# Optimization experiments

Hardware: AMD Instinct MI355X
Metric: run time of the kernel (lower is better)

## Reference

```python
import jax, jax.numpy as jnp
import numpy as np
import math

DIM_IN, DIM_OUT, DIM_HID = 128, 128, 512
DEPTH, HEADS, DIM_HEAD, MLP = 6, 8, 64, 2048
INNER = HEADS * DIM_HEAD  # 512


def _inorm(t, eps=1e-5):
    # torch InstanceNorm1d on ((b h), n, d): normalize over last (spatial) dim, biased var, no affine
    m = jnp.mean(t, axis=-1, keepdims=True)
    v = jnp.mean((t - m) ** 2, axis=-1, keepdims=True)
    return (t - m) * jax.lax.rsqrt(v + eps)


def _layernorm(t, g, b, eps=1e-5):
    m = jnp.mean(t, axis=-1, keepdims=True)
    v = jnp.mean((t - m) ** 2, axis=-1, keepdims=True)
    return (t - m) * jax.lax.rsqrt(v + eps) * g + b


def _pos_encoding(n, d):
    pos = jnp.arange(n, dtype=jnp.float32)[:, None]
    div = jnp.exp(jnp.arange(0, d, 2, dtype=jnp.float32) * (-math.log(10000.0) / d))
    pe = jnp.zeros((n, d), dtype=jnp.float32)
    pe = pe.at[:, 0::2].set(jnp.sin(pos * div))
    pe = pe.at[:, 1::2].set(jnp.cos(pos * div))
    return pe


def setup_inputs() -> dict:
    key = jax.random.key(0)
    ks = jax.random.split(key, 16)
    s = 0.02
    return {
        "x": jax.random.normal(ks[0], (4, 64, 4096, 2), jnp.float32),
        "W_emb": jax.random.normal(ks[1], (DIM_IN, DIM_HID), jnp.float32) * s,
        "b_emb": jnp.zeros((DIM_HID,), jnp.float32),
        "ln_g": jnp.ones((DEPTH, DIM_HID), jnp.float32),
        "ln_b": jnp.zeros((DEPTH, DIM_HID), jnp.float32),
        "Wqkv": jax.random.normal(ks[2], (DEPTH, DIM_HID, 3 * INNER), jnp.float32) * s,
        "Wout": jax.random.normal(ks[3], (DEPTH, INNER, DIM_HID), jnp.float32) * s,
        "b_out": jnp.zeros((DEPTH, DIM_HID), jnp.float32),
        "W1": jax.random.normal(ks[4], (DEPTH, DIM_HID, 2 * MLP), jnp.float32) * s,
        "b1": jnp.zeros((DEPTH, 2 * MLP), jnp.float32),
        "W2": jax.random.normal(ks[5], (DEPTH, MLP, DIM_HID), jnp.float32) * s,
        "b2": jnp.zeros((DEPTH, DIM_HID), jnp.float32),
        "Wd": jax.random.normal(ks[6], (DIM_HID, DIM_OUT), jnp.float32) * s,
        "bd": jnp.zeros((DIM_OUT,), jnp.float32),
    }


def reference(x, W_emb, b_emb, ln_g, ln_b, Wqkv, Wout, b_out, W1, b1, W2, b2, Wd, bd):
    b, t, n, c = x.shape
    h = x.transpose(0, 2, 1, 3).reshape(b, n, t * c)        # [b, n, dim_in]
    h = (h @ W_emb + b_emb) * math.sqrt(DIM_HID)
    h = h + _pos_encoding(n, DIM_HID)[None]                 # positional encoding (dropout=0)
    inv_n = 1.0 / n
    for i in range(DEPTH):
        # PreNorm(LinearAttention) + residual
        y = _layernorm(h, ln_g[i], ln_b[i])
        qkv = y @ Wqkv[i]                                   # [b, n, 3*inner]
        q, k, v = jnp.split(qkv, 3, axis=-1)
        sp = lambda z: z.reshape(b, n, HEADS, DIM_HEAD).transpose(0, 2, 1, 3)  # b h n d
        q, k, v = sp(q), sp(k), sp(v)
        k, v = _inorm(k), _inorm(v)                         # galerkin: norm K and V
        dots = jnp.einsum('bhnd,bhne->bhde', k, v)          # k^T v: O(n) attention
        o = jnp.einsum('bhnd,bhde->bhne', q, dots) * inv_n
        o = o.transpose(0, 2, 1, 3).reshape(b, n, INNER)
        h = o @ Wout[i] + b_out[i] + h
        # FeedForward (no PreNorm in galerkin branch) + residual
        f = h @ W1[i] + b1[i]
        f = jax.nn.gelu(f[..., :MLP], approximate=False) * f[..., MLP:]
        h = f @ W2[i] + b2[i] + h
    out = h @ Wd + bd                                       # [b, n, dim_out]
    return out.transpose(0, 2, 1).reshape(b, -1, 1)         # [b, dim_out*n, 1]
```

## Files before the change

kernel.cpp:

```cpp
#include <hip/hip_runtime.h>
#include <hip/hip_bf16.h>
#include <stdint.h>
#include <math.h>


typedef _Float16 f16x8 __attribute__((ext_vector_type(8)));
typedef float f32x4 __attribute__((ext_vector_type(4)));
typedef unsigned short u16x8 __attribute__((ext_vector_type(8)));
typedef unsigned short u16;

#define SEQ 4096
#define NTOK 16384
#define HID 512
#define RSCL 256.0f
#define RSCLI (1.0f/256.0f)

__device__ __forceinline__ float wred(float x) {
#pragma unroll
  for (int off = 32; off; off >>= 1) x += __shfl_xor(x, off);
  return x;
}

__device__ __forceinline__ u16 f2h(float v) {
  _Float16 h = (_Float16)v;
  return __builtin_bit_cast(u16, h);
}
__device__ __forceinline__ float h2f(u16 u) {
  return (float)__builtin_bit_cast(_Float16, u);
}

__device__ __forceinline__ void gload16(const void* g, void* l) {
  __builtin_amdgcn_global_load_lds(
      reinterpret_cast<const __attribute__((address_space(1))) int*>(
          reinterpret_cast<uintptr_t>(g)),
      reinterpret_cast<__attribute__((address_space(3))) int*>(
          reinterpret_cast<uintptr_t>(l)),
      16, 0, 0);
}

__global__ __launch_bounds__(256) void k_transpose(const float* __restrict__ src,
                                                   u16* __restrict__ dst,
                                                   int K, int N) {
  int d = blockIdx.z;
  const float* s = src + (size_t)d * K * N;
  u16* o = dst + (size_t)d * N * K;
  int k0 = blockIdx.x * 64, n0 = blockIdx.y * 64;
  __shared__ float tile[64][65];
  int t = threadIdx.x, c = t & 63, r4 = t >> 6;
#pragma unroll
  for (int i = 0; i < 16; ++i) {
    int r = i * 4 + r4;
    tile[r][c] = s[(size_t)(k0 + r) * N + n0 + c];
  }
  __syncthreads();
#pragma unroll
  for (int i = 0; i < 16; ++i) {
    int r = i * 4 + r4;
    o[(size_t)(n0 + r) * K + k0 + c] = f2h(tile[c][r]);
  }
}

__global__ __launch_bounds__(256) void k_packx(const float* __restrict__ x,
                                               u16* __restrict__ XP) {
  int idx = blockIdx.x * 256 + threadIdx.x;
  int k = idx & 127, row = idx >> 7;
  int b = row >> 12, n = row & 4095;
  int tt = k >> 1, c = k & 1;
  XP[idx] = f2h(x[(((size_t)(b * 64 + tt)) * SEQ + n) * 2 + c]);
}

__global__ __launch_bounds__(256) void k_ln(const float* __restrict__ H,
                                            const float* __restrict__ G,
                                            const float* __restrict__ B,
                                            u16* __restrict__ Y) {
  int t = threadIdx.x, lane = t & 63;
  int row = blockIdx.x * 4 + (t >> 6);
  const float4* h4 = (const float4*)(H + (size_t)row * HID);
  float4 a = h4[lane * 2], b = h4[lane * 2 + 1];
  float v[8] = {a.x, a.y, a.z, a.w, b.x, b.y, b.z, b.w};
  float s = v[0] + v[1] + v[2] + v[3] + v[4] + v[5] + v[6] + v[7];
  s = wred(s);
  float m = s * (1.0f / 512.0f);
  float q = 0.f;
#pragma unroll
  for (int i = 0; i < 8; ++i) {
    v[i] -= m;
    q += v[i] * v[i];
  }
  q = wred(q);
  float rs = rsqrtf(q * (1.0f / 512.0f) + 1e-5f);
  const float4* g4 = (const float4*)G;
  const float4* b4 = (const float4*)B;
  float4 g1 = g4[lane * 2], g2 = g4[lane * 2 + 1];
  float4 e1 = b4[lane * 2], e2 = b4[lane * 2 + 1];
  float gg[8] = {g1.x, g1.y, g1.z, g1.w, g2.x, g2.y, g2.z, g2.w};
  float ee[8] = {e1.x, e1.y, e1.z, e1.w, e2.x, e2.y, e2.z, e2.w};
  union { u16x8 v; u16 s_[8]; } uh;
#pragma unroll
  for (int i = 0; i < 8; ++i) uh.s_[i] = f2h(v[i] * rs * gg[i] + ee[i]);
  *reinterpret_cast<u16x8*>((u16*)Y + (size_t)row * HID + lane * 8) = uh.v;
}

__global__ __launch_bounds__(256) void k_dots(const u16* __restrict__ QKV,
                                              float* __restrict__ DOTSP) {
  int bh = blockIdx.y, b = bh >> 3, h = bh & 7;
  int n0 = blockIdx.x * 512;
  __shared__ alignas(16) short ks[64 * 64];
  __shared__ alignas(16) short vs[64 * 64];
  int t = threadIdx.x;
  int d0 = (t & 15) * 4, e0 = (t >> 4) * 4;
  float acc[4][4] = {};
  for (int sub = 0; sub < 8; ++sub) {
    int nb = n0 + sub * 64;
#pragma unroll
    for (int i = 0; i < 2; ++i) {
      int c = t + i * 256;
      int r = c >> 3, off = (c & 7) << 3;
      const u16* base = QKV + (size_t)(b * SEQ + nb + r) * 1536;
      gload16(base + 512 + h * 64 + off, ks + c * 8);
      gload16(base + 1024 + h * 64 + off, vs + c * 8);
    }
    asm volatile("s_waitcnt vmcnt(0)" ::: "memory");
    __syncthreads();
    for (int r = 0; r < 64; ++r) {
      short4 kk = *(const short4*)&ks[r * 64 + d0];
      short4 vv = *(const short4*)&vs[r * 64 + e0];
      float kf[4] = {h2f((u16)kk.x), h2f((u16)kk.y), h2f((u16)kk.z), h2f((u16)kk.w)};
      float vf[4] = {h2f((u16)vv.x), h2f((u16)vv.y), h2f((u16)vv.z), h2f((u16)vv.w)};
#pragma unroll
      for (int i = 0; i < 4; ++i)
#pragma unroll
        for (int j = 0; j < 4; ++j) acc[i][j] += kf[i] * vf[j];
    }
    __syncthreads();
  }
  float* dst = DOTSP + ((size_t)blockIdx.x * 32 + bh) * 4096;
#pragma unroll
  for (int i = 0; i < 4; ++i)
#pragma unroll
    for (int j = 0; j < 4; ++j) dst[(d0 + i) * 64 + e0 + j] = acc[i][j];
}

__global__ __launch_bounds__(256) void k_reddots(const float* __restrict__ P,
                                                 float* __restrict__ D) {
  int i = blockIdx.x * 256 + threadIdx.x;
  float s = 0.f;
#pragma unroll
  for (int c = 0; c < 8; ++c) s += P[(size_t)c * 131072 + i];
  D[i] = s;
}

__global__ __launch_bounds__(256) void k_ov(const u16* __restrict__ QKV,
                                            const float* __restrict__ DOTS,
                                            u16* __restrict__ O) {
  int bh = blockIdx.y, b = bh >> 3, h = bh & 7;
  int n0 = blockIdx.x * 64;
  __shared__ alignas(16) float ds[64 * 64];
  __shared__ alignas(16) short qs[64 * 64];
  int t = threadIdx.x;
  const float* dsrc = DOTS + (size_t)bh * 4096;
#pragma unroll
  for (int i = 0; i < 16; ++i) ds[t + i * 256] = dsrc[t + i * 256];
#pragma unroll
  for (int i = 0; i < 2; ++i) {
    int c = t + i * 256, r = c >> 3, off = (c & 7) << 3;
    gload16(QKV + (size_t)(b * SEQ + n0 + r) * 1536 + h * 64 + off, qs + c * 8);
  }
  asm volatile("s_waitcnt vmcnt(0)" ::: "memory");
  __syncthreads();
  int wv = t >> 6, lane = t & 63;
  for (int tok = wv; tok < 64; tok += 4) {
    float acc = 0.f;
#pragma unroll
    for (int d = 0; d < 64; d += 4) {
      short4 q4 = *(const short4*)&qs[tok * 64 + d];
      acc += h2f((u16)q4.x) * ds[(d + 0) * 64 + lane];
      acc += h2f((u16)q4.y) * ds[(d + 1) * 64 + lane];
      acc += h2f((u16)q4.z) * ds[(d + 2) * 64 + lane];
      acc += h2f((u16)q4.w) * ds[(d + 3) * 64 + lane];
    }
    O[(size_t)(b * SEQ + n0 + tok) * 512 + h * 64 + lane] = f2h(acc * (1.0f / SEQ));
  }
}

__device__ __forceinline__ void stage_t(const u16* g, int ldk, int rowBase,
                                        int k0, short* lds, int t) {
#pragma unroll
  for (int i = 0; i < 2; ++i) {
    int c = t + i * 256;
    int r = c >> 2, ko = (c & 3) << 3;
    gload16(g + (size_t)(rowBase + r) * ldk + k0 + ko, lds + c * 8);
  }
}

template <int MODE>
__global__ __launch_bounds__(256, 2) void k_gemm(
    const u16* __restrict__ A, const u16* __restrict__ B1,
    const u16* __restrict__ B2, int K,
    const float* __restrict__ bias, const float* __restrict__ Hin,
    float ascale, float* __restrict__ out32, u16* __restrict__ o16, int ldo) {
  constexpr bool GATED = (MODE == 5);
  constexpr int NTILE = GATED ? 3 : 2;
  __shared__ alignas(16) short sm[2][NTILE][128 * 32];
  const int t = threadIdx.x, lane = t & 63;
  const int wv = t >> 6, wr = wv >> 1, wc = wv & 1;
  const int r16 = lane & 15, grp = lane >> 4;
  const int mBase = blockIdx.y * 128, nBase = blockIdx.x * 128;
  const int NT = K >> 5;

  f32x4 acc[4][4] = {};
  f32x4 acc2[GATED ? 4 : 1][GATED ? 4 : 1] = {};

  auto stage_all = [&](int sb, int k0) {
    stage_t(A, K, mBase, k0, &sm[sb][0][0], t);
    stage_t(B1, K, nBase, k0, &sm[sb][1][0], t);
    if constexpr (GATED) stage_t(B2, K, nBase, k0, &sm[sb][2][0], t);
  };

  stage_all(0, 0);
  asm volatile("s_waitcnt vmcnt(0)" ::: "memory");
  __syncthreads();

  int buf = 0;
  for (int kt = 0; kt < NT; ++kt) {
    if (kt + 1 < NT) stage_all(buf ^ 1, (kt + 1) << 5);
    const int fo = grp * 8;
    f16x8 af[4], b1v[4];
#pragma unroll
    for (int f = 0; f < 4; ++f)
      af[f] = *(const f16x8*)&sm[buf][0][(wr * 64 + f * 16 + r16) * 32 + fo];
#pragma unroll
    for (int f = 0; f < 4; ++f)
      b1v[f] = *(const f16x8*)&sm[buf][1][(wc * 64 + f * 16 + r16) * 32 + fo];
#pragma unroll
    for (int i = 0; i < 4; ++i)
#pragma unroll
      for (int j = 0; j < 4; ++j)
        acc[i][j] = __builtin_amdgcn_mfma_f32_16x16x32_f16(af[i], b1v[j], acc[i][j], 0, 0, 0);
    if constexpr (GATED) {
      f16x8 b2v[4];
#pragma unroll
      for (int f = 0; f < 4; ++f)
        b2v[f] = *(const f16x8*)&sm[buf][2][(wc * 64 + f * 16 + r16) * 32 + fo];
#pragma unroll
      for (int i = 0; i < 4; ++i)
#pragma unroll
        for (int j = 0; j < 4; ++j)
          acc2[i][j] = __builtin_amdgcn_mfma_f32_16x16x32_f16(af[i], b2v[j], acc2[i][j], 0, 0, 0);
    }
    if (kt + 1 < NT) {
      asm volatile("s_waitcnt vmcnt(0)" ::: "memory");
      __syncthreads();
      buf ^= 1;
    }
  }

  if constexpr (MODE == 1) {
    const bool doNorm = (nBase >= 512);
#pragma unroll
    for (int i = 0; i < 4; ++i) {
#pragma unroll
      for (int r = 0; r < 4; ++r) {
        float s = 0.f, s2 = 0.f;
#pragma unroll
        for (int j = 0; j < 4; ++j) {
          float v = acc[i][j][r];
          s += v;
          s2 += v * v;
        }
#pragma unroll
        for (int off = 8; off; off >>= 1) {
          s += __shfl_xor(s, off);
          s2 += __shfl_xor(s2, off);
        }
        float m = s * (1.0f / 64.0f);
        float var = fmaxf(s2 * (1.0f / 64.0f) - m * m, 0.f);
        float rs = rsqrtf(var + 1e-5f);
        int row = mBase + wr * 64 + i * 16 + grp * 4 + r;
#pragma unroll
        for (int j = 0; j < 4; ++j) {
          int col = nBase + wc * 64 + j * 16 + r16;
          float v = acc[i][j][r];
          if (doNorm) v = (v - m) * rs;
          o16[(size_t)row * ldo + col] = f2h(v);
        }
      }
    }
    return;
  }

#pragma unroll
  for (int i = 0; i < 4; ++i) {
#pragma unroll
    for (int j = 0; j < 4; ++j) {
#pragma unroll
      for (int r = 0; r < 4; ++r) {
        int row = mBase + wr * 64 + i * 16 + grp * 4 + r;
        int col = nBase + wc * 64 + j * 16 + r16;
        float v = acc[i][j][r];
        if constexpr (MODE == 0) {
          v = (v + bias[col]) * 22.627416997969522f;
          int n = row & (SEQ - 1);
          int k2 = col >> 1;
          float ang = (float)n * expf((float)k2 * -0.03597789207803197f);
          v += (col & 1) ? cosf(ang) : sinf(ang);
          out32[(size_t)row * HID + col] = v;
        } else if constexpr (MODE == 2) {
          v = v * ascale + bias[col] + Hin[(size_t)row * HID + col];
          out32[(size_t)row * HID + col] = v;
          o16[(size_t)row * HID + col] = f2h(v * RSCLI);
        } else if constexpr (MODE == 7) {
          v = v * RSCL + bias[col];
          out32[(size_t)(row >> 12) * (128 * 4096) + (size_t)col * SEQ + (row & 4095)] = v;
        } else {
          float a = v * RSCL + bias[col];
          float c2 = acc2[i][j][r] * RSCL + bias[2048 + col];
          float gl = 0.5f * a * (1.0f + erff(a * 0.7071067811865475f));
          o16[(size_t)row * ldo + col] = f2h(gl * c2 * RSCLI);
        }
      }
    }
  }
}

extern "C" void kernel_launch(void* const* d_in, const int* in_sizes, int n_in,
                              void* d_out, int out_size, void* d_ws, size_t ws_size,
                              hipStream_t stream) {
  const float* x    = (const float*)d_in[0];
  const float* Wemb = (const float*)d_in[1];
  const float* bemb = (const float*)d_in[2];
  const float* lng  = (const float*)d_in[3];
  const float* lnb  = (const float*)d_in[4];
  const float* Wqkv = (const float*)d_in[5];
  const float* Wout = (const float*)d_in[6];
  const float* bout = (const float*)d_in[7];
  const float* W1   = (const float*)d_in[8];
  const float* b1   = (const float*)d_in[9];
  const float* W2   = (const float*)d_in[10];
  const float* b2   = (const float*)d_in[11];
  const float* Wd   = (const float*)d_in[12];
  const float* bd   = (const float*)d_in[13];

  char* p = (char*)d_ws;
  auto alloc = [&](size_t bytes) {
    char* r = p;
    p += (bytes + 255) & ~(size_t)255;
    return r;
  };
  u16* WembT = (u16*)alloc((size_t)512 * 128 * 2);
  u16* WqkvT = (u16*)alloc((size_t)6 * 1536 * 512 * 2);
  u16* WoutT = (u16*)alloc((size_t)6 * 512 * 512 * 2);
  u16* W1T   = (u16*)alloc((size_t)6 * 4096 * 512 * 2);
  u16* W2T   = (u16*)alloc((size_t)6 * 512 * 2048 * 2);
  u16* WdT   = (u16*)alloc((size_t)128 * 512 * 2);
  float* H   = (float*)alloc((size_t)NTOK * 512 * 4);
  u16* HB    = (u16*)alloc((size_t)NTOK * 512 * 2);
  float* DOTSP = (float*)alloc((size_t)8 * 32 * 4096 * 4);
  float* DOTS  = (float*)alloc((size_t)32 * 4096 * 4);
  char* U = alloc((size_t)64 * 1024 * 1024);
  const size_t MI = 1024 * 1024;
  u16* XP  = (u16*)U;
  u16* Y   = (u16*)U;
  u16* QKV = (u16*)(U + 16 * MI);
  u16* O   = (u16*)U;
  u16* F   = (u16*)U;

  k_transpose<<<dim3(2, 8, 1),  256, 0, stream>>>(Wemb, WembT, 128, 512);
  k_transpose<<<dim3(8, 24, 6), 256, 0, stream>>>(Wqkv, WqkvT, 512, 1536);
  k_transpose<<<dim3(8, 8, 6),  256, 0, stream>>>(Wout, WoutT, 512, 512);
  k_transpose<<<dim3(8, 64, 6), 256, 0, stream>>>(W1, W1T, 512, 4096);
  k_transpose<<<dim3(32, 8, 6), 256, 0, stream>>>(W2, W2T, 2048, 512);
  k_transpose<<<dim3(8, 2, 1),  256, 0, stream>>>(Wd, WdT, 512, 128);

  k_packx<<<8192, 256, 0, stream>>>(x, XP);
  k_gemm<0><<<dim3(4, 128), 256, 0, stream>>>(XP, WembT, nullptr, 128, bemb,
      nullptr, 1.f, H, nullptr, 0);

  for (int i = 0; i < 6; ++i) {
    k_ln<<<4096, 256, 0, stream>>>(H, lng + i * 512, lnb + i * 512, Y);
    k_gemm<1><<<dim3(12, 128), 256, 0, stream>>>(Y,
        WqkvT + (size_t)i * 1536 * 512, nullptr, 512,
        nullptr, nullptr, 1.f, nullptr, QKV, 1536);
    k_dots<<<dim3(8, 32), 256, 0, stream>>>(QKV, DOTSP);
    k_reddots<<<512, 256, 0, stream>>>(DOTSP, DOTS);
    k_ov<<<dim3(64, 32), 256, 0, stream>>>(QKV, DOTS, O);
    k_gemm<2><<<dim3(4, 128), 256, 0, stream>>>(O,
        WoutT + (size_t)i * 512 * 512, nullptr, 512,
        bout + i * 512, H, 1.f, H, HB, 512);
    k_gemm<5><<<dim3(16, 128), 256, 0, stream>>>(HB,
        W1T + (size_t)i * 4096 * 512,
        W1T + (size_t)i * 4096 * 512 + (size_t)2048 * 512, 512,
        b1 + i * 4096, nullptr, 1.f, nullptr, F, 2048);
    k_gemm<2><<<dim3(4, 128), 256, 0, stream>>>(F,
        W2T + (size_t)i * 512 * 2048, nullptr, 2048,
        b2 + i * 512, H, RSCL, H, HB, 512);
  }
  k_gemm<7><<<dim3(1, 128), 256, 0, stream>>>(HB, WdT, nullptr, 512, bd,
      nullptr, 1.f, (float*)d_out, nullptr, 0);
}
```

Baseline: 1.911 ms.

## Restructure GEMM pipeline with swizzled LDS, deeper prefetch, and dedicated gated-FFN kernel

Rewrites the GEMM main loop to prefetch two K-tiles ahead, using partial vmcnt waits and raw barriers instead of a full drain every iteration. LDS tiles get an XOR swizzle to cut bank conflicts, and occupancy hints rise to 4 blocks. The gated FFN GEMM moves to a separate 512-thread kernel with a 128x256 tile that shares A fragments across both weight halves. That kernel replaces the exact erf GELU with a tanh approximation built on __expf. This approximation changes the numerics away from the exact GELU the reference uses.

After: 5.291 ms. +176.9%, slower.

```diff
diff --git a/kernel.cpp b/kernel.cpp
--- a/kernel.cpp
+++ b/kernel.cpp
@@ -27,6 +27,13 @@
 }
 __device__ __forceinline__ float h2f(u16 u) {
   return (float)__builtin_bit_cast(_Float16, u);
+}
+
+__device__ __forceinline__ float fgelu(float a) {
+  float t = 0.7978845608f * a * (1.0f + 0.044715f * a * a);
+  float e = __expf(2.0f * t);
+  float th = 1.0f - 2.0f / (e + 1.0f);
+  return 0.5f * a * (1.0f + th);
 }
 
 __device__ __forceinline__ void gload16(const void* g, void* l) {
@@ -36,6 +43,18 @@
       reinterpret_cast<__attribute__((address_space(3))) int*>(
           reinterpret_cast<uintptr_t>(l)),
       16, 0, 0);
+}
+
+__device__ __forceinline__ void stS(const u16* g, int ldk, int rowBase, int k0,
+                                    short* lds, int c) {
+  int pr = c >> 3, s8 = (c & 7) ^ (pr & 7);
+  int r = pr * 2 + (s8 >> 2);
+  gload16(g + (size_t)(rowBase + r) * ldk + k0 + (s8 & 3) * 8, lds + c * 8);
+}
+__device__ __forceinline__ int idxg(int row, int grp) {
+  int pr = row >> 1;
+  int s8 = ((((row & 1) << 2) | grp) ^ (pr & 7));
+  return pr * 64 + s8 * 8;
 }
 
 __global__ __launch_bounds__(256) void k_transpose(const float* __restrict__ src,
@@ -183,25 +202,12 @@
   }
 }
 
-__device__ __forceinline__ void stage_t(const u16* g, int ldk, int rowBase,
-                                        int k0, short* lds, int t) {
-#pragma unroll
-  for (int i = 0; i < 2; ++i) {
-    int c = t + i * 256;
-    int r = c >> 2, ko = (c & 3) << 3;
-    gload16(g + (size_t)(rowBase + r) * ldk + k0 + ko, lds + c * 8);
-  }
-}
-
 template <int MODE>
-__global__ __launch_bounds__(256, 2) void k_gemm(
-    const u16* __restrict__ A, const u16* __restrict__ B1,
-    const u16* __restrict__ B2, int K,
+__global__ __launch_bounds__(256, 4) void k_gemm(
+    const u16* __restrict__ A, const u16* __restrict__ B1, int K,
     const float* __restrict__ bias, const float* __restrict__ Hin,
     float ascale, float* __restrict__ out32, u16* __restrict__ o16, int ldo) {
-  constexpr bool GATED = (MODE == 5);
-  constexpr int NTILE = GATED ? 3 : 2;
-  __shared__ alignas(16) short sm[2][NTILE][128 * 32];
+  __shared__ alignas(16) short sm[2][2][4096];
   const int t = threadIdx.x, lane = t & 63;
   const int wv = t >> 6, wr = wv >> 1, wc = wv & 1;
   const int r16 = lane & 15, grp = lane >> 4;
@@ -209,50 +215,40 @@
   const int NT = K >> 5;
 
   f32x4 acc[4][4] = {};
-  f32x4 acc2[GATED ? 4 : 1][GATED ? 4 : 1] = {};
 
   auto stage_all = [&](int sb, int k0) {
-    stage_t(A, K, mBase, k0, &sm[sb][0][0], t);
-    stage_t(B1, K, nBase, k0, &sm[sb][1][0], t);
-    if constexpr (GATED) stage_t(B2, K, nBase, k0, &sm[sb][2][0], t);
+    stS(A, K, mBase, k0, &sm[sb][0][0], t);
+    stS(A, K, mBase, k0, &sm[sb][0][0], t + 256);
+    stS(B1, K, nBase, k0, &sm[sb][1][0], t);
+    stS(B1, K, nBase, k0, &sm[sb][1][0], t + 256);
   };
 
   stage_all(0, 0);
-  asm volatile("s_waitcnt vmcnt(0)" ::: "memory");
-  __syncthreads();
-
-  int buf = 0;
+  stage_all(1, 32);
+
   for (int kt = 0; kt < NT; ++kt) {
-    if (kt + 1 < NT) stage_all(buf ^ 1, (kt + 1) << 5);
-    const int fo = grp * 8;
-    f16x8 af[4], b1v[4];
+    const int cur = kt & 1;
+    if (kt + 1 < NT) asm volatile("s_waitcnt vmcnt(4)" ::: "memory");
+    else             asm volatile("s_waitcnt vmcnt(0)" ::: "memory");
+    __builtin_amdgcn_s_barrier();
+    f16x8 af[4], bv[4];
 #pragma unroll
     for (int f = 0; f < 4; ++f)
-      af[f] = *(const f16x8*)&sm[buf][0][(wr * 64 + f * 16 + r16) * 32 + fo];
+      af[f] = *(const f16x8*)&sm[cur][0][idxg(wr * 64 + f * 16 + r16, grp)];
 #pragma unroll
     for (int f = 0; f < 4; ++f)
-      b1v[f] = *(const f16x8*)&sm[buf][1][(wc * 64 + f * 16 + r16) * 32 + fo];
+      bv[f] = *(const f16x8*)&sm[cur][1][idxg(wc * 64 + f * 16 + r16, grp)];
+    asm volatile("s_waitcnt lgkmcnt(0)" ::: "memory");
+    __builtin_amdgcn_sched_barrier(0);
+    __builtin_amdgcn_s_barrier();
+    if (kt + 2 < NT) stage_all(cur, (kt + 2) << 5);
+    __builtin_amdgcn_s_setprio(1);
 #pragma unroll
     for (int i = 0; i < 4; ++i)
 #pragma unroll
       for (int j = 0; j < 4; ++j)
-        acc[i][j] = __builtin_amdgcn_mfma_f32_16x16x32_f16(af[i], b1v[j], acc[i][j], 0, 0, 0);
-    if constexpr (GATED) {
-      f16x8 b2v[4];
-#pragma unroll
-      for (int f = 0; f < 4; ++f)
-        b2v[f] = *(const f16x8*)&sm[buf][2][(wc * 64 + f * 16 + r16) * 32 + fo];
-#pragma unroll
-      for (int i = 0; i < 4; ++i)
-#pragma unroll
-        for (int j = 0; j < 4; ++j)
-          acc2[i][j] = __builtin_amdgcn_mfma_f32_16x16x32_f16(af[i], b2v[j], acc2[i][j], 0, 0, 0);
-    }
-    if (kt + 1 < NT) {
-      asm volatile("s_waitcnt vmcnt(0)" ::: "memory");
-      __syncthreads();
-      buf ^= 1;
-    }
+        acc[i][j] = __builtin_amdgcn_mfma_f32_16x16x32_f16(af[i], bv[j], acc[i][j], 0, 0, 0);
+    __builtin_amdgcn_s_setprio(0);
   }
 
   if constexpr (MODE == 1) {
@@ -309,15 +305,81 @@
           v = v * ascale + bias[col] + Hin[(size_t)row * HID + col];
           out32[(size_t)row * HID + col] = v;
           o16[(size_t)row * HID + col] = f2h(v * RSCLI);
-        } else if constexpr (MODE == 7) {
+        } else {
           v = v * RSCL + bias[col];
           out32[(size_t)(row >> 12) * (128 * 4096) + (size_t)col * SEQ + (row & 4095)] = v;
-        } else {
-          float a = v * RSCL + bias[col];
-          float c2 = acc2[i][j][r] * RSCL + bias[2048 + col];
-          float gl = 0.5f * a * (1.0f + erff(a * 0.7071067811865475f));
-          o16[(size_t)row * ldo + col] = f2h(gl * c2 * RSCLI);
         }
+      }
+    }
+  }
+}
+
+__global__ __launch_bounds__(512, 4) void k_gemmG(
+    const u16* __restrict__ A, int lda,
+    const u16* __restrict__ B1, const u16* __restrict__ B2, int K,
+    const float* __restrict__ bias, u16* __restrict__ o16, int ldo) {
+  __shared__ alignas(16) short sm[2][20480];
+  const int t = threadIdx.x, lane = t & 63;
+  const int w = t >> 6, wr = w >> 2, wcn = w & 3;
+  const int r16 = lane & 15, grp = lane >> 4;
+  const int mBase = blockIdx.y * 128, nBase = blockIdx.x * 256;
+  const int NT = K >> 5;
+
+  f32x4 acc[4][4] = {};
+  f32x4 acc2[4][4] = {};
+
+  auto stage_all = [&](int sb, int k0) {
+    stS(A, lda, mBase, k0, &sm[sb][0], t);
+    stS(B1, K, nBase, k0, &sm[sb][4096], t);
+    stS(B1, K, nBase, k0, &sm[sb][4096], t + 512);
+    stS(B2, K, nBase, k0, &sm[sb][12288], t);
+    stS(B2, K, nBase, k0, &sm[sb][12288], t + 512);
+  };
+
+  stage_all(0, 0);
+  stage_all(1, 32);
+
+  for (int kt = 0; kt < NT; ++kt) {
+    const int cur = kt & 1;
+    if (kt + 1 < NT) asm volatile("s_waitcnt vmcnt(5)" ::: "memory");
+    else             asm volatile("s_waitcnt vmcnt(0)" ::: "memory");
+    __builtin_amdgcn_s_barrier();
+    f16x8 af[4], b1v[4], b2v[4];
+#pragma unroll
+    for (int i = 0; i < 4; ++i)
+      af[i] = *(const f16x8*)&sm[cur][idxg(wr * 64 + i * 16 + r16, grp)];
+#pragma unroll
+    for (int j = 0; j < 4; ++j) {
+      int ro = idxg(wcn * 64 + j * 16 + r16, grp);
+      b1v[j] = *(const f16x8*)&sm[cur][4096 + ro];
+      b2v[j] = *(const f16x8*)&sm[cur][12288 + ro];
+    }
+    asm volatile("s_waitcnt lgkmcnt(0)" ::: "memory");
+    __builtin_amdgcn_sched_barrier(0);
+    __builtin_amdgcn_s_barrier();
+    if (kt + 2 < NT) stage_all(cur, (kt + 2) << 5);
+    __builtin_amdgcn_s_setprio(1);
+#pragma unroll
+    for (int i = 0; i < 4; ++i)
+#pragma unroll
+      for (int j = 0; j < 4; ++j) {
+        acc[i][j] = __builtin_amdgcn_mfma_f32_16x16x32_f16(af[i], b1v[j], acc[i][j], 0, 0, 0);
+        acc2[i][j] = __builtin_amdgcn_mfma_f32_16x16x32_f16(af[i], b2v[j], acc2[i][j], 0, 0, 0);
+      }
+    __builtin_amdgcn_s_setprio(0);
+  }
+
+#pragma unroll
+  for (int i = 0; i < 4; ++i) {
+#pragma unroll
+    for (int j = 0; j < 4; ++j) {
+#pragma unroll
+      for (int r = 0; r < 4; ++r) {
+        int row = mBase + wr * 64 + i * 16 + grp * 4 + r;
+        int col = nBase + wcn * 64 + j * 16 + r16;
+        float a = acc[i][j][r] * RSCL + bias[col];
+        float c2 = acc2[i][j][r] * RSCL + bias[2048 + col];
+        o16[(size_t)row * ldo + col] = f2h(fgelu(a) * c2 * RSCLI);
       }
     }
   }
@@ -373,28 +435,26 @@
   k_transpose<<<dim3(8, 2, 1),  256, 0, stream>>>(Wd, WdT, 512, 128);
 
   k_packx<<<8192, 256, 0, stream>>>(x, XP);
-  k_gemm<0><<<dim3(4, 128), 256, 0, stream>>>(XP, WembT, nullptr, 128, bemb,
+  k_gemm<0><<<dim3(4, 128), 256, 0, stream>>>(XP, WembT, 128, bemb,
       nullptr, 1.f, H, nullptr, 0);
 
   for (int i = 0; i < 6; ++i) {
     k_ln<<<4096, 256, 0, stream>>>(H, lng + i * 512, lnb + i * 512, Y);
     k_gemm<1><<<dim3(12, 128), 256, 0, stream>>>(Y,
-        WqkvT + (size_t)i * 1536 * 512, nullptr, 512,
-        nullptr, nullptr, 1.f, nullptr, QKV, 1536);
+        WqkvT + (size_t)i * 1536 * 512, 512, nullptr, nullptr, 1.f,
+        nullptr, QKV, 1536);
     k_dots<<<dim3(8, 32), 256, 0, stream>>>(QKV, DOTSP);
     k_reddots<<<512, 256, 0, stream>>>(DOTSP, DOTS);
     k_ov<<<dim3(64, 32), 256, 0, stream>>>(QKV, DOTS, O);
     k_gemm<2><<<dim3(4, 128), 256, 0, stream>>>(O,
-        WoutT + (size_t)i * 512 * 512, nullptr, 512,
-        bout + i * 512, H, 1.f, H, HB, 512);
-    k_gemm<5><<<dim3(16, 128), 256, 0, stream>>>(HB,
+        WoutT + (size_t)i * 512 * 512, 512, bout + i * 512, H, 1.f, H, HB, 512);
+    k_gemmG<<<dim3(8, 128), 512, 0, stream>>>(HB, 512,
         W1T + (size_t)i * 4096 * 512,
         W1T + (size_t)i * 4096 * 512 + (size_t)2048 * 512, 512,
-        b1 + i * 4096, nullptr, 1.f, nullptr, F, 2048);
+        b1 + i * 4096, F, 2048);
     k_gemm<2><<<dim3(4, 128), 256, 0, stream>>>(F,
-        W2T + (size_t)i * 512 * 2048, nullptr, 2048,
-        b2 + i * 512, H, RSCL, H, HB, 512);
-  }
-  k_gemm<7><<<dim3(1, 128), 256, 0, stream>>>(HB, WdT, nullptr, 512, bd,
+        W2T + (size_t)i * 512 * 2048, 2048, b2 + i * 512, H, RSCL, H, HB, 512);
+  }
+  k_gemm<7><<<dim3(1, 128), 256, 0, stream>>>(HB, WdT, 512, bd,
       nullptr, 1.f, (float*)d_out, nullptr, 0);
 }
```
